# Kernel optimization log

Measured on AMD Instinct MI355X. Metric: run time of the kernel, lower is better.

The kernel has to match this reference:

```python
import jax, jax.numpy as jnp
import numpy as np

HEADS = 8
WS = 8


def setup_inputs() -> dict:
    key = jax.random.key(0)
    k1, k2, k3, k4 = jax.random.split(key, 4)
    C = 256
    x = jax.random.normal(k1, (4, C, 256, 256), dtype=jnp.float32)
    w_qkv = jax.random.normal(k2, (3 * C, C), dtype=jnp.float32) * (C ** -0.5)
    w_out = jax.random.normal(k3, (C, C), dtype=jnp.float32) * (C ** -0.5)
    b_out = jax.random.normal(k4, (C,), dtype=jnp.float32) * 0.02
    return {"x": x, "w_qkv": w_qkv, "w_out": w_out, "b_out": b_out}


def reference(x, w_qkv, w_out, b_out):
    B, C, H, W = x.shape
    ws, heads = WS, HEADS
    d = C // heads
    scale = d ** -0.5
    pad_h = (ws - H % ws) % ws
    pad_w = (ws - W % ws) % ws
    xp = jnp.pad(x, ((0, 0), (0, 0), (0, pad_h), (0, pad_w)))
    Hp, Wp = H + pad_h, W + pad_w
    nh, nw = Hp // ws, Wp // ws
    # b c (nh wh) (nw ww) -> (b nh nw) c wh ww
    xw = xp.reshape(B, C, nh, ws, nw, ws).transpose(0, 2, 4, 1, 3, 5)
    xw = xw.reshape(B * nh * nw, C, ws, ws)
    # 1x1 conv qkv projection (bias-free): [3C,C] x [Bw,C,h,w]
    qkv = jnp.einsum('oc,bchw->bohw', w_qkv, xw)
    q, k, v = jnp.split(qkv, 3, axis=1)

    def to_heads(t):
        # b (h d) x y -> b h (x y) d
        Bw = t.shape[0]
        return t.reshape(Bw, heads, d, ws * ws).transpose(0, 1, 3, 2)

    q, k, v = to_heads(q), to_heads(k), to_heads(v)
    attn = jnp.einsum('bhid,bhjd->bhij', q, k) * scale
    attn = jax.nn.softmax(attn, axis=-1)
    out = jnp.einsum('bhij,bhjd->bhid', attn, v)
    # b h (x y) d -> b (h d) x y
    Bw = out.shape[0]
    out = out.transpose(0, 1, 3, 2).reshape(Bw, C, ws, ws)
    out = jnp.einsum('oc,bchw->bohw', w_out, out) + b_out[None, :, None, None]
    # (b nh nw) c wh ww -> b c (nh wh) (nw ww)
    out = out.reshape(B, nh, nw, C, ws, ws).transpose(0, 3, 1, 4, 2, 5)
    out = out.reshape(B, C, Hp, Wp)
    return out[:, :, :H, :W]
```

## Files before the change

kernel.cpp:

```cpp
#include <hip/hip_runtime.h>

typedef __attribute__((ext_vector_type(4))) float f32x4;
typedef __attribute__((ext_vector_type(8))) short bf16x8;
typedef __attribute__((ext_vector_type(4))) unsigned int u32x4;

#define MFMA32 __builtin_amdgcn_mfma_f32_16x16x32_bf16

__device__ __forceinline__ unsigned short f2bf(float f) {
  unsigned int u = __float_as_uint(f);
  return (unsigned short)((u + 0x7FFFu + ((u >> 16) & 1u)) >> 16);
}
__device__ __forceinline__ unsigned int pack2(float a, float b) {
  return (unsigned int)f2bf(a) | ((unsigned int)f2bf(b) << 16);
}
__device__ __forceinline__ bf16x8 mk8(unsigned int a, unsigned int b,
                                      unsigned int c, unsigned int d) {
  u32x4 u = {a, b, c, d};
  return __builtin_bit_cast(bf16x8, u);
}
__device__ __forceinline__ int xsw(int tok, int cb) {
  return (tok * 512 + cb) ^ ((((tok >> 3) ^ tok) & 7) << 4);
}

__global__ void convw_kernel(const float* __restrict__ wqkv,
                             const float* __restrict__ wout,
                             unsigned short* __restrict__ dst) {
  int i = blockIdx.x * 256 + threadIdx.x;
  if (i < 196608) dst[i] = f2bf(wqkv[i]);
  if (i < 65536) dst[196608 + i] = f2bf(wout[i]);
}

__global__ __launch_bounds__(256, 2) void wattn_kernel(
    const float* __restrict__ x, const unsigned short* __restrict__ wqkv,
    const unsigned short* __restrict__ wout, const float* __restrict__ bo,
    float* __restrict__ y) {
  __shared__ __align__(16) char lds[32768];

  const int tid = threadIdx.x;
  const int l = tid & 63;
  const int w = tid >> 6;
  const int lo = l & 15;
  const int dg = l >> 4;

  const int bid = blockIdx.x;
  const int rw = ((bid & 7) << 9) | (bid >> 3);
  const int b = rw >> 10;
  const int rem = rw & 1023;
  const int wy = rem >> 5;
  const int wx = rem & 31;

  const size_t wbase = ((size_t)b * 65536 + (size_t)wy * 8) * 256 + (size_t)wx * 8;
  const float* xw = x + wbase;
  float* yw = y + wbase;

  {
    const int irow = lo >> 1;
    const int jq = lo & 1;
    const float* xp = xw + irow * 256 + jq * 4;
    const int tok0 = irow * 8 + jq * 4;
#pragma unroll
    for (int cc = 0; cc < 4; ++cc) {
      const int cb = w * 64 + cc * 16 + dg * 4;
      f32x4 v0 = *(const f32x4*)(xp + (size_t)(cb + 0) * 65536);
      f32x4 v1 = *(const f32x4*)(xp + (size_t)(cb + 1) * 65536);
      f32x4 v2 = *(const f32x4*)(xp + (size_t)(cb + 2) * 65536);
      f32x4 v3 = *(const f32x4*)(xp + (size_t)(cb + 3) * 65536);
#pragma unroll
      for (int t = 0; t < 4; ++t) {
        uint2 uu;
        uu.x = pack2(v0[t], v1[t]);
        uu.y = pack2(v2[t], v3[t]);
        *(uint2*)(lds + xsw(tok0 + t, cb * 2)) = uu;
      }
    }
  }
  __syncthreads();

  const float lscale = 0.17677669529663687f * 1.4426950408889634f;

  unsigned int outp[2][2][4][2];

#pragma unroll
  for (int hh = 0; hh < 2; ++hh) {
    const int h = w * 2 + hh;
    const unsigned short* wp = wqkv + (size_t)(h * 32 + lo) * 256 + dg * 8;

    bf16x8 qf[4], kf[4];
    {
      f32x4 qa[2][4];
#pragma unroll
      for (int a = 0; a < 2; ++a)
#pragma unroll
        for (int it = 0; it < 4; ++it) qa[a][it] = {0.f, 0.f, 0.f, 0.f};
#pragma unroll
      for (int kk = 0; kk < 8; ++kk) {
        bf16x8 xf[4];
#pragma unroll
        for (int it = 0; it < 4; ++it)
          xf[it] = *(const bf16x8*)(lds + xsw(it * 16 + lo, kk * 64 + dg * 16));
        bf16x8 wq0 = *(const bf16x8*)(wp + kk * 32);
        bf16x8 wq1 = *(const bf16x8*)(wp + 4096 + kk * 32);
#pragma unroll
        for (int it = 0; it < 4; ++it) {
          qa[0][it] = MFMA32(wq0, xf[it], qa[0][it], 0, 0, 0);
          qa[1][it] = MFMA32(wq1, xf[it], qa[1][it], 0, 0, 0);
        }
      }
#pragma unroll
      for (int it = 0; it < 4; ++it)
        qf[it] = mk8(pack2(qa[0][it][0], qa[0][it][1]), pack2(qa[0][it][2], qa[0][it][3]),
                     pack2(qa[1][it][0], qa[1][it][1]), pack2(qa[1][it][2], qa[1][it][3]));
    }
    {
      f32x4 ka[2][4];
#pragma unroll
      for (int a = 0; a < 2; ++a)
#pragma unroll
        for (int it = 0; it < 4; ++it) ka[a][it] = {0.f, 0.f, 0.f, 0.f};
#pragma unroll
      for (int kk = 0; kk < 8; ++kk) {
        bf16x8 xf[4];
#pragma unroll
        for (int it = 0; it < 4; ++it)
          xf[it] = *(const bf16x8*)(lds + xsw(it * 16 + lo, kk * 64 + dg * 16));
        bf16x8 wk0 = *(const bf16x8*)(wp + 65536 + kk * 32);
        bf16x8 wk1 = *(const bf16x8*)(wp + 69632 + kk * 32);
#pragma unroll
        for (int it = 0; it < 4; ++it) {
          ka[0][it] = MFMA32(wk0, xf[it], ka[0][it], 0, 0, 0);
          ka[1][it] = MFMA32(wk1, xf[it], ka[1][it], 0, 0, 0);
        }
      }
#pragma unroll
      for (int it = 0; it < 4; ++it)
        kf[it] = mk8(pack2(ka[0][it][0], ka[0][it][1]), pack2(ka[0][it][2], ka[0][it][3]),
                     pack2(ka[1][it][0], ka[1][it][1]), pack2(ka[1][it][2], ka[1][it][3]));
    }
    bf16x8 vf[2][2];
    {
      f32x4 va[4][2];
#pragma unroll
      for (int tb = 0; tb < 4; ++tb)
#pragma unroll
        for (int dt = 0; dt < 2; ++dt) va[tb][dt] = {0.f, 0.f, 0.f, 0.f};
#pragma unroll
      for (int kk = 0; kk < 8; ++kk) {
        bf16x8 xf[4];
#pragma unroll
        for (int tb = 0; tb < 4; ++tb)
          xf[tb] = *(const bf16x8*)(lds + xsw(tb * 16 + lo, kk * 64 + dg * 16));
        bf16x8 wv0 = *(const bf16x8*)(wp + 131072 + kk * 32);
        bf16x8 wv1 = *(const bf16x8*)(wp + 135168 + kk * 32);
#pragma unroll
        for (int tb = 0; tb < 4; ++tb) {
          va[tb][0] = MFMA32(xf[tb], wv0, va[tb][0], 0, 0, 0);
          va[tb][1] = MFMA32(xf[tb], wv1, va[tb][1], 0, 0, 0);
        }
      }
#pragma unroll
      for (int sb = 0; sb < 2; ++sb)
#pragma unroll
        for (int dt = 0; dt < 2; ++dt)
          vf[sb][dt] = mk8(pack2(va[2 * sb][dt][0], va[2 * sb][dt][1]),
                           pack2(va[2 * sb][dt][2], va[2 * sb][dt][3]),
                           pack2(va[2 * sb + 1][dt][0], va[2 * sb + 1][dt][1]),
                           pack2(va[2 * sb + 1][dt][2], va[2 * sb + 1][dt][3]));
    }

#pragma unroll
    for (int it = 0; it < 4; ++it) {
      f32x4 stt[4];
#pragma unroll
      for (int jt = 0; jt < 4; ++jt) {
        f32x4 z = {0.f, 0.f, 0.f, 0.f};
        stt[jt] = MFMA32(kf[jt], qf[it], z, 0, 0, 0);
      }
      float m = stt[0][0];
#pragma unroll
      for (int jt = 0; jt < 4; ++jt)
#pragma unroll
        for (int t = 0; t < 4; ++t) m = fmaxf(m, stt[jt][t]);
      m = fmaxf(m, __shfl_xor(m, 16, 64));
      m = fmaxf(m, __shfl_xor(m, 32, 64));
      const float mls = m * lscale;
      float s = 0.f;
#pragma unroll
      for (int jt = 0; jt < 4; ++jt)
#pragma unroll
        for (int t = 0; t < 4; ++t) {
          float e = exp2f(fmaf(stt[jt][t], lscale, -mls));
          stt[jt][t] = e;
          s += e;
        }
      s += __shfl_xor(s, 16, 64);
      s += __shfl_xor(s, 32, 64);
      const float rs = 1.0f / s;

      bf16x8 pp0 = mk8(pack2(stt[0][0], stt[0][1]), pack2(stt[0][2], stt[0][3]),
                       pack2(stt[1][0], stt[1][1]), pack2(stt[1][2], stt[1][3]));
      bf16x8 pp1 = mk8(pack2(stt[2][0], stt[2][1]), pack2(stt[2][2], stt[2][3]),
                       pack2(stt[3][0], stt[3][1]), pack2(stt[3][2], stt[3][3]));
#pragma unroll
      for (int dt = 0; dt < 2; ++dt) {
        f32x4 z = {0.f, 0.f, 0.f, 0.f};
        f32x4 o = MFMA32(vf[0][dt], pp0, z, 0, 0, 0);
        o = MFMA32(vf[1][dt], pp1, o, 0, 0, 0);
        o *= rs;
        outp[hh][dt][it][0] = pack2(o[0], o[1]);
        outp[hh][dt][it][1] = pack2(o[2], o[3]);
      }
    }
  }

  __syncthreads();

#pragma unroll
  for (int hh = 0; hh < 2; ++hh) {
    const int h = w * 2 + hh;
#pragma unroll
    for (int dt = 0; dt < 2; ++dt)
#pragma unroll
      for (int it = 0; it < 4; ++it) {
        uint2 uu;
        uu.x = outp[hh][dt][it][0];
        uu.y = outp[hh][dt][it][1];
        *(uint2*)(lds + xsw(it * 16 + lo, h * 64 + dt * 32 + dg * 8)) = uu;
      }
  }
  __syncthreads();

#pragma unroll
  for (int oh = 0; oh < 2; ++oh) {
    const unsigned short* wo0 =
        wout + (size_t)(w * 64 + oh * 32 + lo) * 256 + dg * 8;
    f32x4 ya[2][4];
#pragma unroll
    for (int ot = 0; ot < 2; ++ot)
#pragma unroll
      for (int it = 0; it < 4; ++it) ya[ot][it] = {0.f, 0.f, 0.f, 0.f};
#pragma unroll
    for (int kk = 0; kk < 8; ++kk) {
      bf16x8 bt[4];
#pragma unroll
      for (int it = 0; it < 4; ++it)
        bt[it] = *(const bf16x8*)(lds + xsw(it * 16 + lo, kk * 64 + dg * 16));
      bf16x8 wf0 = *(const bf16x8*)(wo0 + kk * 32);
      bf16x8 wf1 = *(const bf16x8*)(wo0 + 4096 + kk * 32);
#pragma unroll
      for (int it = 0; it < 4; ++it) {
        ya[0][it] = MFMA32(bt[it], wf0, ya[0][it], 0, 0, 0);
        ya[1][it] = MFMA32(bt[it], wf1, ya[1][it], 0, 0, 0);
      }
    }
#pragma unroll
    for (int ot = 0; ot < 2; ++ot) {
      const int orow = w * 64 + oh * 32 + ot * 16 + lo;
      const float bv = bo[orow];
#pragma unroll
      for (int it = 0; it < 4; ++it) {
        f32x4 r = ya[ot][it];
        r[0] += bv; r[1] += bv; r[2] += bv; r[3] += bv;
        const int tok0 = it * 16 + dg * 4;
        *(f32x4*)(yw + (size_t)orow * 65536 +
                  (size_t)(tok0 >> 3) * 256 + (tok0 & 7)) = r;
      }
    }
  }
}

extern "C" void kernel_launch(void* const* d_in, const int* in_sizes, int n_in,
                              void* d_out, int out_size, void* d_ws, size_t ws_size,
                              hipStream_t stream) {
  const float* x = (const float*)d_in[0];
  const float* wqkv = (const float*)d_in[1];
  const float* wout = (const float*)d_in[2];
  const float* bo = (const float*)d_in[3];
  float* y = (float*)d_out;
  unsigned short* wbf = (unsigned short*)d_ws;

  convw_kernel<<<768, 256, 0, stream>>>(wqkv, wout, wbf);
  wattn_kernel<<<4096, 256, 0, stream>>>(x, wbf, wbf + 196608, bo, y);
}
```

Baseline: 398.9 us.

## Split fused window attention into attention and output-projection kernels via workspace

The single fused kernel becomes two. The first computes QKV and attention, writes the bf16 per-window attention output to a global workspace buffer, and launches with higher occupancy bounds. The second reads that buffer back, re-swizzles it into LDS, and applies the output projection plus bias. The aim is to lower register pressure and raise occupancy in each stage, at the cost of an extra 128MB of global traffic and a second launch. A monolithic fallback is kept for when the workspace is too small.

```diff
diff --git a/kernel.cpp b/kernel.cpp
--- a/kernel.cpp
+++ b/kernel.cpp
@@ -20,6 +20,10 @@
 }
 __device__ __forceinline__ int xsw(int tok, int cb) {
   return (tok * 512 + cb) ^ ((((tok >> 3) ^ tok) & 7) << 4);
+}
+__device__ __forceinline__ int winid() {
+  const int bid = blockIdx.x;
+  return ((bid & 7) << 9) | (bid >> 3);
 }
 
 __global__ void convw_kernel(const float* __restrict__ wqkv,
@@ -30,10 +34,9 @@
   if (i < 65536) dst[196608 + i] = f2bf(wout[i]);
 }
 
-__global__ __launch_bounds__(256, 2) void wattn_kernel(
+__global__ __launch_bounds__(256, 3) void wattnA_kernel(
     const float* __restrict__ x, const unsigned short* __restrict__ wqkv,
-    const unsigned short* __restrict__ wout, const float* __restrict__ bo,
-    float* __restrict__ y) {
+    unsigned short* __restrict__ abuf) {
   __shared__ __align__(16) char lds[32768];
 
   const int tid = threadIdx.x;
@@ -42,16 +45,13 @@
   const int lo = l & 15;
   const int dg = l >> 4;
 
-  const int bid = blockIdx.x;
-  const int rw = ((bid & 7) << 9) | (bid >> 3);
+  const int rw = winid();
   const int b = rw >> 10;
   const int rem = rw & 1023;
   const int wy = rem >> 5;
   const int wx = rem & 31;
-
   const size_t wbase = ((size_t)b * 65536 + (size_t)wy * 8) * 256 + (size_t)wx * 8;
   const float* xw = x + wbase;
-  float* yw = y + wbase;
 
   {
     const int irow = lo >> 1;
@@ -78,12 +78,11 @@
 
   const float lscale = 0.17677669529663687f * 1.4426950408889634f;
 
-  unsigned int outp[2][2][4][2];
-
 #pragma unroll
   for (int hh = 0; hh < 2; ++hh) {
     const int h = w * 2 + hh;
     const unsigned short* wp = wqkv + (size_t)(h * 32 + lo) * 256 + dg * 8;
+    unsigned short* ap = abuf + (size_t)rw * 16384 + h * 2048;
 
     bf16x8 qf[4], kf[4];
     {
@@ -196,6 +195,266 @@
       s += __shfl_xor(s, 32, 64);
       const float rs = 1.0f / s;
 
+      bf16x8 pp0 = mk8(pack2(stt[0][0], stt[0][1]), pack2(stt[0][2], stt[0][3]),
+                       pack2(stt[1][0], stt[1][1]), pack2(stt[1][2], stt[1][3]));
+      bf16x8 pp1 = mk8(pack2(stt[2][0], stt[2][1]), pack2(stt[2][2], stt[2][3]),
+                       pack2(stt[3][0], stt[3][1]), pack2(stt[3][2], stt[3][3]));
+#pragma unroll
+      for (int dt = 0; dt < 2; ++dt) {
+        f32x4 z = {0.f, 0.f, 0.f, 0.f};
+        f32x4 o = MFMA32(vf[0][dt], pp0, z, 0, 0, 0);
+        o = MFMA32(vf[1][dt], pp1, o, 0, 0, 0);
+        o *= rs;
+        uint2 uu;
+        uu.x = pack2(o[0], o[1]);
+        uu.y = pack2(o[2], o[3]);
+        *(uint2*)(ap + it * 512 + dt * 256 + dg * 64 + lo * 4) = uu;
+      }
+    }
+  }
+}
+
+__global__ __launch_bounds__(256, 4) void projB_kernel(
+    const unsigned short* __restrict__ abuf, const unsigned short* __restrict__ wout,
+    const float* __restrict__ bo, float* __restrict__ y) {
+  __shared__ __align__(16) char lds[32768];
+
+  const int tid = threadIdx.x;
+  const int l = tid & 63;
+  const int w = tid >> 6;
+  const int lo = l & 15;
+  const int dg = l >> 4;
+
+  const int rw = winid();
+  const int b = rw >> 10;
+  const int rem = rw & 1023;
+  const int wy = rem >> 5;
+  const int wx = rem & 31;
+  const size_t wbase = ((size_t)b * 65536 + (size_t)wy * 8) * 256 + (size_t)wx * 8;
+  float* yw = y + wbase;
+
+  {
+    const unsigned short* ap = abuf + (size_t)rw * 16384;
+#pragma unroll
+    for (int j = 0; j < 8; ++j) {
+      const int e0 = j * 2048 + tid * 8;
+      u32x4 v = *(const u32x4*)(ap + e0);
+      const int h = e0 >> 11;
+      const int r = e0 & 2047;
+      const int it_ = r >> 9;
+      const int dt_ = (r >> 8) & 1;
+      const int dg_ = (r >> 6) & 3;
+      const int lo2 = (r >> 2) & 15;
+      const int tok = it_ * 16 + lo2;
+      const int cb = h * 64 + dt_ * 32 + dg_ * 8;
+      uint2 a0, a1;
+      a0.x = v[0]; a0.y = v[1];
+      a1.x = v[2]; a1.y = v[3];
+      *(uint2*)(lds + xsw(tok, cb)) = a0;
+      *(uint2*)(lds + xsw(tok + 1, cb)) = a1;
+    }
+  }
+  __syncthreads();
+
+#pragma unroll
+  for (int oh = 0; oh < 2; ++oh) {
+    const unsigned short* wo0 =
+        wout + (size_t)(w * 64 + oh * 32 + lo) * 256 + dg * 8;
+    f32x4 ya[2][4];
+#pragma unroll
+    for (int ot = 0; ot < 2; ++ot)
+#pragma unroll
+      for (int it = 0; it < 4; ++it) ya[ot][it] = {0.f, 0.f, 0.f, 0.f};
+#pragma unroll
+    for (int kk = 0; kk < 8; ++kk) {
+      bf16x8 bt[4];
+#pragma unroll
+      for (int it = 0; it < 4; ++it)
+        bt[it] = *(const bf16x8*)(lds + xsw(it * 16 + lo, kk * 64 + dg * 16));
+      bf16x8 wf0 = *(const bf16x8*)(wo0 + kk * 32);
+      bf16x8 wf1 = *(const bf16x8*)(wo0 + 4096 + kk * 32);
+#pragma unroll
+      for (int it = 0; it < 4; ++it) {
+        ya[0][it] = MFMA32(bt[it], wf0, ya[0][it], 0, 0, 0);
+        ya[1][it] = MFMA32(bt[it], wf1, ya[1][it], 0, 0, 0);
+      }
+    }
+#pragma unroll
+    for (int ot = 0; ot < 2; ++ot) {
+      const int orow = w * 64 + oh * 32 + ot * 16 + lo;
+      const float bv = bo[orow];
+#pragma unroll
+      for (int it = 0; it < 4; ++it) {
+        f32x4 r = ya[ot][it];
+        r[0] += bv; r[1] += bv; r[2] += bv; r[3] += bv;
+        const int tok0 = it * 16 + dg * 4;
+        *(f32x4*)(yw + (size_t)orow * 65536 +
+                  (size_t)(tok0 >> 3) * 256 + (tok0 & 7)) = r;
+      }
+    }
+  }
+}
+
+__global__ __launch_bounds__(256, 2) void wattn_mono(
+    const float* __restrict__ x, const unsigned short* __restrict__ wqkv,
+    const unsigned short* __restrict__ wout, const float* __restrict__ bo,
+    float* __restrict__ y) {
+  __shared__ __align__(16) char lds[32768];
+
+  const int tid = threadIdx.x;
+  const int l = tid & 63;
+  const int w = tid >> 6;
+  const int lo = l & 15;
+  const int dg = l >> 4;
+
+  const int rw = winid();
+  const int b = rw >> 10;
+  const int rem = rw & 1023;
+  const int wy = rem >> 5;
+  const int wx = rem & 31;
+  const size_t wbase = ((size_t)b * 65536 + (size_t)wy * 8) * 256 + (size_t)wx * 8;
+  const float* xw = x + wbase;
+  float* yw = y + wbase;
+
+  {
+    const int irow = lo >> 1;
+    const int jq = lo & 1;
+    const float* xp = xw + irow * 256 + jq * 4;
+    const int tok0 = irow * 8 + jq * 4;
+#pragma unroll
+    for (int cc = 0; cc < 4; ++cc) {
+      const int cb = w * 64 + cc * 16 + dg * 4;
+      f32x4 v0 = *(const f32x4*)(xp + (size_t)(cb + 0) * 65536);
+      f32x4 v1 = *(const f32x4*)(xp + (size_t)(cb + 1) * 65536);
+      f32x4 v2 = *(const f32x4*)(xp + (size_t)(cb + 2) * 65536);
+      f32x4 v3 = *(const f32x4*)(xp + (size_t)(cb + 3) * 65536);
+#pragma unroll
+      for (int t = 0; t < 4; ++t) {
+        uint2 uu;
+        uu.x = pack2(v0[t], v1[t]);
+        uu.y = pack2(v2[t], v3[t]);
+        *(uint2*)(lds + xsw(tok0 + t, cb * 2)) = uu;
+      }
+    }
+  }
+  __syncthreads();
+
+  const float lscale = 0.17677669529663687f * 1.4426950408889634f;
+  unsigned int outp[2][2][4][2];
+
+#pragma unroll
+  for (int hh = 0; hh < 2; ++hh) {
+    const int h = w * 2 + hh;
+    const unsigned short* wp = wqkv + (size_t)(h * 32 + lo) * 256 + dg * 8;
+    bf16x8 qf[4], kf[4];
+    {
+      f32x4 qa[2][4];
+#pragma unroll
+      for (int a = 0; a < 2; ++a)
+#pragma unroll
+        for (int it = 0; it < 4; ++it) qa[a][it] = {0.f, 0.f, 0.f, 0.f};
+#pragma unroll
+      for (int kk = 0; kk < 8; ++kk) {
+        bf16x8 xf[4];
+#pragma unroll
+        for (int it = 0; it < 4; ++it)
+          xf[it] = *(const bf16x8*)(lds + xsw(it * 16 + lo, kk * 64 + dg * 16));
+        bf16x8 wq0 = *(const bf16x8*)(wp + kk * 32);
+        bf16x8 wq1 = *(const bf16x8*)(wp + 4096 + kk * 32);
+#pragma unroll
+        for (int it = 0; it < 4; ++it) {
+          qa[0][it] = MFMA32(wq0, xf[it], qa[0][it], 0, 0, 0);
+          qa[1][it] = MFMA32(wq1, xf[it], qa[1][it], 0, 0, 0);
+        }
+      }
+#pragma unroll
+      for (int it = 0; it < 4; ++it)
+        qf[it] = mk8(pack2(qa[0][it][0], qa[0][it][1]), pack2(qa[0][it][2], qa[0][it][3]),
+                     pack2(qa[1][it][0], qa[1][it][1]), pack2(qa[1][it][2], qa[1][it][3]));
+    }
+    {
+      f32x4 ka[2][4];
+#pragma unroll
+      for (int a = 0; a < 2; ++a)
+#pragma unroll
+        for (int it = 0; it < 4; ++it) ka[a][it] = {0.f, 0.f, 0.f, 0.f};
+#pragma unroll
+      for (int kk = 0; kk < 8; ++kk) {
+        bf16x8 xf[4];
+#pragma unroll
+        for (int it = 0; it < 4; ++it)
+          xf[it] = *(const bf16x8*)(lds + xsw(it * 16 + lo, kk * 64 + dg * 16));
+        bf16x8 wk0 = *(const bf16x8*)(wp + 65536 + kk * 32);
+        bf16x8 wk1 = *(const bf16x8*)(wp + 69632 + kk * 32);
+#pragma unroll
+        for (int it = 0; it < 4; ++it) {
+          ka[0][it] = MFMA32(wk0, xf[it], ka[0][it], 0, 0, 0);
+          ka[1][it] = MFMA32(wk1, xf[it], ka[1][it], 0, 0, 0);
+        }
+      }
+#pragma unroll
+      for (int it = 0; it < 4; ++it)
+        kf[it] = mk8(pack2(ka[0][it][0], ka[0][it][1]), pack2(ka[0][it][2], ka[0][it][3]),
+                     pack2(ka[1][it][0], ka[1][it][1]), pack2(ka[1][it][2], ka[1][it][3]));
+    }
+    bf16x8 vf[2][2];
+    {
+      f32x4 va[4][2];
+#pragma unroll
+      for (int tb = 0; tb < 4; ++tb)
+#pragma unroll
+        for (int dt = 0; dt < 2; ++dt) va[tb][dt] = {0.f, 0.f, 0.f, 0.f};
+#pragma unroll
+      for (int kk = 0; kk < 8; ++kk) {
+        bf16x8 xf[4];
+#pragma unroll
+        for (int tb = 0; tb < 4; ++tb)
+          xf[tb] = *(const bf16x8*)(lds + xsw(tb * 16 + lo, kk * 64 + dg * 16));
+        bf16x8 wv0 = *(const bf16x8*)(wp + 131072 + kk * 32);
+        bf16x8 wv1 = *(const bf16x8*)(wp + 135168 + kk * 32);
+#pragma unroll
+        for (int tb = 0; tb < 4; ++tb) {
+          va[tb][0] = MFMA32(xf[tb], wv0, va[tb][0], 0, 0, 0);
+          va[tb][1] = MFMA32(xf[tb], wv1, va[tb][1], 0, 0, 0);
+        }
+      }
+#pragma unroll
+      for (int sb = 0; sb < 2; ++sb)
+#pragma unroll
+        for (int dt = 0; dt < 2; ++dt)
+          vf[sb][dt] = mk8(pack2(va[2 * sb][dt][0], va[2 * sb][dt][1]),
+                           pack2(va[2 * sb][dt][2], va[2 * sb][dt][3]),
+                           pack2(va[2 * sb + 1][dt][0], va[2 * sb + 1][dt][1]),
+                           pack2(va[2 * sb + 1][dt][2], va[2 * sb + 1][dt][3]));
+    }
+#pragma unroll
+    for (int it = 0; it < 4; ++it) {
+      f32x4 stt[4];
+#pragma unroll
+      for (int jt = 0; jt < 4; ++jt) {
+        f32x4 z = {0.f, 0.f, 0.f, 0.f};
+        stt[jt] = MFMA32(kf[jt], qf[it], z, 0, 0, 0);
+      }
+      float m = stt[0][0];
+#pragma unroll
+      for (int jt = 0; jt < 4; ++jt)
+#pragma unroll
+        for (int t = 0; t < 4; ++t) m = fmaxf(m, stt[jt][t]);
+      m = fmaxf(m, __shfl_xor(m, 16, 64));
+      m = fmaxf(m, __shfl_xor(m, 32, 64));
+      const float mls = m * lscale;
+      float s = 0.f;
+#pragma unroll
+      for (int jt = 0; jt < 4; ++jt)
+#pragma unroll
+        for (int t = 0; t < 4; ++t) {
+          float e = exp2f(fmaf(stt[jt][t], lscale, -mls));
+          stt[jt][t] = e;
+          s += e;
+        }
+      s += __shfl_xor(s, 16, 64);
+      s += __shfl_xor(s, 32, 64);
+      const float rs = 1.0f / s;
       bf16x8 pp0 = mk8(pack2(stt[0][0], stt[0][1]), pack2(stt[0][2], stt[0][3]),
                        pack2(stt[1][0], stt[1][1]), pack2(stt[1][2], stt[1][3]));
       bf16x8 pp1 = mk8(pack2(stt[2][0], stt[2][1]), pack2(stt[2][2], stt[2][3]),
@@ -211,9 +470,7 @@
       }
     }
   }
-
   __syncthreads();
-
 #pragma unroll
   for (int hh = 0; hh < 2; ++hh) {
     const int h = w * 2 + hh;
@@ -228,7 +485,6 @@
       }
   }
   __syncthreads();
-
 #pragma unroll
   for (int oh = 0; oh < 2; ++oh) {
     const unsigned short* wo0 =
@@ -279,5 +535,13 @@
   unsigned short* wbf = (unsigned short*)d_ws;
 
   convw_kernel<<<768, 256, 0, stream>>>(wqkv, wout, wbf);
-  wattn_kernel<<<4096, 256, 0, stream>>>(x, wbf, wbf + 196608, bo, y);
-}
+
+  const size_t need = 524288 + (size_t)4096 * 16384 * 2;
+  if (ws_size >= need) {
+    unsigned short* abuf = wbf + 262144;
+    wattnA_kernel<<<4096, 256, 0, stream>>>(x, wbf, abuf);
+    projB_kernel<<<4096, 256, 0, stream>>>(abuf, wbf + 196608, bo, y);
+  } else {
+    wattn_mono<<<4096, 256, 0, stream>>>(x, wbf, wbf + 196608, bo, y);
+  }
+}
```

New measurement: 633.0 us. 58.7% more time.
